# Performance work log

Hardware: AMD Instinct MI355X
Metric: run time of the kernel (lower is better)

## Reference

```python
import jax, jax.numpy as jnp
import numpy as np

D_MODEL = 1024
N_HEADS = 16
D_K = D_MODEL // N_HEADS  # 64
N_CLASSES = 32
S_LEN = 16   # synonyms per class
BATCH = 32
T_LEN = 512  # key/value sequence length


def setup_inputs() -> dict:
    key = jax.random.key(0)
    k1, k2, k3, k4, k5, k6 = jax.random.split(key, 6)
    Q = jax.random.normal(k1, (N_CLASSES, S_LEN, D_MODEL), dtype=jnp.float32)
    H = jax.random.normal(k2, (BATCH, T_LEN, D_MODEL), dtype=jnp.float32)
    ql = jax.random.normal(k3, (N_CLASSES, D_MODEL), dtype=jnp.float32)
    # torch Linear weights are (out_features, in_features), init N(0, 0.001)
    WQ_w = 0.001 * jax.random.normal(k4, (D_MODEL, D_MODEL), dtype=jnp.float32)
    WK_w = 0.001 * jax.random.normal(k5, (D_MODEL, D_MODEL), dtype=jnp.float32)
    WV_w = 0.001 * jax.random.normal(k6, (D_MODEL, D_MODEL), dtype=jnp.float32)
    return {"Q": Q, "H": H, "ql": ql, "WQ_w": WQ_w, "WK_w": WK_w, "WV_w": WV_w}


def reference(Q, H, ql, WQ_w, WK_w, WV_w):
    c, s, d = Q.shape
    b, t, _ = H.shape
    nh, dk = N_HEADS, D_K
    # projections (torch Linear: x @ W.T)
    q_s = (Q @ WQ_w.T).reshape(c, s, nh, dk).transpose(0, 2, 1, 3)   # czsh
    k_s = (H @ WK_w.T).reshape(b, t, nh, dk).transpose(0, 2, 1, 3)   # bzth
    Wql = ql @ WV_w.T                                                # ch
    Hh = H.reshape(b, t, nh, dk).transpose(0, 2, 1, 3)               # bzth
    WK = jnp.tanh(k_s)
    K = jnp.tanh(Hh)
    # scores: (b, c, z, s, t)
    scores = jnp.einsum('bzth,czsh->bczst', WK, q_s)
    attn = jax.nn.softmax(scores, axis=-1)
    # context: (b, c, z, s, h)
    context = jnp.einsum('bzth,bczst->bczsh', K, attn)
    # AvgPool3d((1, s, 1)) + squeeze(-2): mean over s -> (b, c, z, h)
    ctx = context.mean(axis=3).reshape(b, c, nh * dk)                # (b, c, d_model)
    output = jnp.einsum('bch,ch->bc', ctx, Wql)
    return output
```

## Files before the change

### kernel.cpp

```cpp
#include <hip/hip_runtime.h>
#include <hip/hip_bf16.h>
#include <math.h>

#define D_MODEL 1024
#define N_HEADS 16
#define D_K 64
#define N_CLASSES 32
#define S_LEN 16
#define BATCH 32
#define T_LEN 512

typedef __bf16 bf16_t;
typedef bf16_t bf16x8 __attribute__((ext_vector_type(8)));
typedef float f32x4 __attribute__((ext_vector_type(4)));
typedef long lx2 __attribute__((ext_vector_type(2)));

__device__ inline unsigned short f2bf(float f) {
    unsigned int u = __float_as_uint(f);
    unsigned int r = (u + 0x7FFFu + ((u >> 16) & 1u)) >> 16;
    return (unsigned short)r;
}
__device__ inline float fast_tanh(float x) {
    float e = __expf(2.0f * x);
    return (e - 1.0f) * __builtin_amdgcn_rcpf(e + 1.0f);
}
__device__ inline float4 fast_tanh4(float4 v) {
    return make_float4(fast_tanh(v.x), fast_tanh(v.y), fast_tanh(v.z), fast_tanh(v.w));
}
__device__ inline float dot4(float4 a, float4 b) {
    return a.x * b.x + a.y * b.y + a.z * b.z + a.w * b.w;
}
__device__ inline float exp2_fast(float x) {
    float r;
    asm("v_exp_f32 %0, %1" : "=v"(r) : "v"(x));
    return r;
}
__device__ inline int pack_fp8x4(float4 v) {
    int p = __builtin_amdgcn_cvt_pk_fp8_f32(v.x, v.y, 0, false);
    p = __builtin_amdgcn_cvt_pk_fp8_f32(v.z, v.w, p, true);
    return p;
}
__device__ inline bf16x8 bf8_from_f32(const float* p) {
    float4 a = *(const float4*)p;
    float4 b = *(const float4*)(p + 4);
    union { bf16x8 v; unsigned short s[8]; } u;
    u.s[0] = f2bf(a.x); u.s[1] = f2bf(a.y); u.s[2] = f2bf(a.z); u.s[3] = f2bf(a.w);
    u.s[4] = f2bf(b.x); u.s[5] = f2bf(b.y); u.s[6] = f2bf(b.z); u.s[7] = f2bf(b.w);
    return u.v;
}

__device__ inline void async16(void* lds, const void* g) {
    __builtin_amdgcn_global_load_lds(
        (const __attribute__((address_space(1))) unsigned int*)g,
        (__attribute__((address_space(3))) unsigned int*)lds, 16, 0, 0);
}

__global__ __launch_bounds__(256) void prep_kernel(
    const float* __restrict__ H, int* __restrict__ Hf8,
    const float* __restrict__ WK, int* __restrict__ WKf8,
    const float4* __restrict__ Q, ushort4* __restrict__ Qb,
    const float4* __restrict__ WQ, ushort4* __restrict__ WQb,
    const float* __restrict__ ql, const float* __restrict__ WV,
    float* __restrict__ wql)
{
    __shared__ __align__(16) char psm[25600];
    const int bid = blockIdx.x;
    const int tid = threadIdx.x;
    if (bid < 256) {
        float4 (*qls)[16] = (float4(*)[16])psm;
        float4 (*WVs)[17] = (float4(*)[17])(psm + 8192);
        const int n0 = (bid & 15) * 64;
        const int k0 = (bid >> 4) * 64;
        for (int i = tid; i < 512; i += 256)
            qls[i >> 4][i & 15] = *(const float4*)(ql + (size_t)(i >> 4) * D_MODEL + k0 + (i & 15) * 4);
        for (int i = tid; i < 1024; i += 256)
            WVs[i >> 4][i & 15] = *(const float4*)(WV + (size_t)(n0 + (i >> 4)) * D_MODEL + k0 + (i & 15) * 4);
        __syncthreads();

        const int n = tid & 63;
        const int c0 = (tid >> 6) * 8;
        float acc[8] = {};
        for (int kq = 0; kq < 16; kq++) {
            const float4 wv = WVs[n][kq];
#pragma unroll
            for (int c = 0; c < 8; c++) acc[c] += dot4(qls[c0 + c][kq], wv);
        }
#pragma unroll
        for (int c = 0; c < 8; c++)
            atomicAdd(&wql[(size_t)(c0 + c) * D_MODEL + n0 + n], acc[c]);
    } else if (bid < 17664) {
        int i = (bid - 256) * 256 + tid;
        const float* in; int* out; float s;
        if (i < 4194304) { in = H; out = Hf8; s = 1.0f; }
        else { i -= 4194304; in = WK; out = WKf8; s = 512.0f; }
        const int p = i << 2;
        const int blk = p >> 10;
        const int pos = p & 1023;
        const int rb = blk >> 4, kb = blk & 15;
        const int q = pos >> 4;
        const int quad = q >> 4, l16 = q & 15;
        const int o = pos & 15;
        const int kh = o >> 3, b0 = o & 7;
        const int r = rb * 16 + l16;
        const int k = kb * 64 + kh * 32 + quad * 8 + b0;
        float4 v = *(const float4*)(in + (size_t)r * 1024 + k);
        v.x *= s; v.y *= s; v.z *= s; v.w *= s;
        out[i] = pack_fp8x4(v);
    } else {
        int i = (bid - 17664) * 256 + tid;
        const float4* in; ushort4* out; float s;
        if (i < 131072) { in = Q + i; out = Qb + i; s = 1.4426950408889634f; }
        else { i -= 131072; in = WQ + i; out = WQb + i; s = 1.0f; }
        float4 v = *in;
        ushort4 o;
        o.x = f2bf(v.x * s); o.y = f2bf(v.y * s); o.z = f2bf(v.z * s); o.w = f2bf(v.w * s);
        *out = o;
    }
}

__global__ __launch_bounds__(256) void gemms_kernel(
    const unsigned char* __restrict__ A8, const unsigned char* __restrict__ B8,
    unsigned short* __restrict__ wkt_b,
    const unsigned short* __restrict__ Qb, const unsigned short* __restrict__ WQb,
    unsigned short* __restrict__ qproj_b,
    const float* __restrict__ H, const float* __restrict__ wql,
    float* __restrict__ kv)
{
    __shared__ __align__(16) char smem[33280];
    const int bid = blockIdx.x;
    const int tid = threadIdx.x;
    const int wid = tid >> 6;
    const int lane = tid & 63;
    const int quad = lane >> 4;
    const int l16 = lane & 15;

    if (bid < 1024) {
        unsigned char* As = (unsigned char*)smem;
        unsigned char* Bs = (unsigned char*)smem + 8192;
        const int m0 = (bid & 127) * 128;
        const int n0 = (bid >> 7) * 128;
        const int wm = (wid >> 1) * 64;
        const int wn = (wid & 1) * 64;
        const int stA = wm >> 4;
        const int stB = wn >> 4;
        const int st = wid;
        const int cl = lane * 16;

        f32x4 acc[4][4] = {};
        const unsigned char* Ab = A8 + ((size_t)(m0 >> 4) * 16) * 1024;
        const unsigned char* Bb = B8 + ((size_t)(n0 >> 4) * 16) * 1024;

        for (int kb = 0; kb < 16; kb++) {
            async16(&As[tid * 16],        Ab + ((size_t)st * 16 + kb) * 1024 + cl);
            async16(&As[4096 + tid * 16], Ab + ((size_t)(st + 4) * 16 + kb) * 1024 + cl);
            async16(&Bs[tid * 16],        Bb + ((size_t)st * 16 + kb) * 1024 + cl);
            async16(&Bs[4096 + tid * 16], Bb + ((size_t)(st + 4) * 16 + kb) * 1024 + cl);
            __syncthreads();

            lx2 a8[4], b8[4];
#pragma unroll
            for (int mt = 0; mt < 4; mt++)
                a8[mt] = *(const lx2*)&As[(stA + mt) * 1024 + lane * 16];
#pragma unroll
            for (int nt = 0; nt < 4; nt++)
                b8[nt] = *(const lx2*)&Bs[(stB + nt) * 1024 + lane * 16];
#pragma unroll
            for (int mt = 0; mt < 4; mt++)
#pragma unroll
                for (int nt = 0; nt < 4; nt++) {
                    acc[mt][nt] = __builtin_amdgcn_mfma_f32_16x16x32_fp8_fp8(
                        a8[mt].x, b8[nt].x, acc[mt][nt], 0, 0, 0);
                    acc[mt][nt] = __builtin_amdgcn_mfma_f32_16x16x32_fp8_fp8(
                        a8[mt].y, b8[nt].y, acc[mt][nt], 0, 0, 0);
                }
            __syncthreads();
        }

#pragma unroll
        for (int mt = 0; mt < 4; mt++)
#pragma unroll
            for (int nt = 0; nt < 4; nt++)
#pragma unroll
                for (int r = 0; r < 4; r++) {
                    const int row = m0 + wm + mt * 16 + quad * 4 + r;
                    const int col = n0 + wn + nt * 16 + l16;
                    wkt_b[(size_t)row * 1024 + col] =
                        f2bf(fast_tanh(acc[mt][nt][r] * (1.0f / 512.0f)));
                }
    } else if (bid < 1056) {
        unsigned short* As = (unsigned short*)smem;
        unsigned short* Bs = (unsigned short*)(smem + 8192);
        const int q = bid - 1024;
        const int m0 = (q & 3) * 128;
        const int n0 = (q >> 2) * 128;
        const int wm = (wid >> 1) * 64;
        const int wn = (wid & 1) * 64;

        f32x4 acc[4][4] = {};
        const int r0 = tid >> 2;
        const int cc0 = (tid & 3) * 8;

        for (int k0 = 0; k0 < 1024; k0 += 32) {
            async16(&As[tid * 8],        Qb  + (size_t)(m0 + r0) * 1024 + k0 + cc0);
            async16(&As[2048 + tid * 8], Qb  + (size_t)(m0 + 64 + r0) * 1024 + k0 + cc0);
            async16(&Bs[tid * 8],        WQb + (size_t)(n0 + r0) * 1024 + k0 + cc0);
            async16(&Bs[2048 + tid * 8], WQb + (size_t)(n0 + 64 + r0) * 1024 + k0 + cc0);
            __syncthreads();

            bf16x8 af[4], bfr[4];
#pragma unroll
            for (int mt = 0; mt < 4; mt++)
                af[mt] = *(const bf16x8*)&As[(wm + mt * 16 + l16) * 32 + quad * 8];
#pragma unroll
            for (int nt = 0; nt < 4; nt++)
                bfr[nt] = *(const bf16x8*)&Bs[(wn + nt * 16 + l16) * 32 + quad * 8];
#pragma unroll
            for (int mt = 0; mt < 4; mt++)
#pragma unroll
                for (int nt = 0; nt < 4; nt++)
                    acc[mt][nt] = __builtin_amdgcn_mfma_f32_16x16x32_bf16(
                        af[mt], bfr[nt], acc[mt][nt], 0, 0, 0);
            __syncthreads();
        }

#pragma unroll
        for (int mt = 0; mt < 4; mt++)
#pragma unroll
            for (int nt = 0; nt < 4; nt++)
#pragma unroll
                for (int r = 0; r < 4; r++) {
                    const int row = m0 + wm + mt * 16 + quad * 4 + r;
                    const int col = n0 + wn + nt * 16 + l16;
                    qproj_b[(size_t)row * 1024 + col] = f2bf(acc[mt][nt][r]);
                }
    } else {
        unsigned short* Ks = (unsigned short*)smem;
        float* kvt = (float*)(smem + 16384);
        const int q = bid - 1056;
        const int chunk = q & 127;
        const int z = q >> 7;
        const int b = chunk >> 2;
        const int t0 = (chunk & 3) * 128;

#pragma unroll
        for (int it = 0; it < 8; it++) {
            const int idx = it * 256 + tid;
            const int row = idx >> 4;
            const int c4 = (idx & 15) * 4;
            float4 v = *(const float4*)(H + ((size_t)b * T_LEN + t0 + row) * D_MODEL + z * D_K + c4);
            v = fast_tanh4(v);
            ushort4 o;
            o.x = f2bf(v.x); o.y = f2bf(v.y); o.z = f2bf(v.z); o.w = f2bf(v.w);
            *(ushort4*)&Ks[row * 64 + c4] = o;
        }
        bf16x8 bfr[2][2];
#pragma unroll
        for (int ct = 0; ct < 2; ct++)
#pragma unroll
            for (int kh = 0; kh < 2; kh++)
                bfr[ct][kh] = bf8_from_f32(wql +
                    (size_t)(ct * 16 + l16) * D_MODEL + z * D_K + kh * 32 + quad * 8);
        __syncthreads();

        const int wt = wid * 32;
        f32x4 acc[2][2] = {};
#pragma unroll
        for (int tt = 0; tt < 2; tt++) {
            const bf16x8 a0 = *(const bf16x8*)&Ks[(wt + tt * 16 + l16) * 64 + quad * 8];
            const bf16x8 a1 = *(const bf16x8*)&Ks[(wt + tt * 16 + l16) * 64 + 32 + quad * 8];
#pragma unroll
            for (int ct = 0; ct < 2; ct++) {
                acc[tt][ct] = __builtin_amdgcn_mfma_f32_16x16x32_bf16(a0, bfr[ct][0], acc[tt][ct], 0, 0, 0);
                acc[tt][ct] = __builtin_amdgcn_mfma_f32_16x16x32_bf16(a1, bfr[ct][1], acc[tt][ct], 0, 0, 0);
            }
        }
#pragma unroll
        for (int tt = 0; tt < 2; tt++)
#pragma unroll
            for (int ct = 0; ct < 2; ct++)
#pragma unroll
                for (int r = 0; r < 4; r++)
                    kvt[(wt + tt * 16 + quad * 4 + r) * 33 + ct * 16 + l16] = acc[tt][ct][r];
        __syncthreads();

        float* outb = kv + (((size_t)b * 16 + z) * 32) * 512 + t0;
#pragma unroll
        for (int it = 0; it < 4; it++) {
            const int idx = it * 256 + tid;
            const int c = idx >> 5;
            const int tq = (idx & 31) * 4;
            float4 v = make_float4(kvt[(tq + 0) * 33 + c], kvt[(tq + 1) * 33 + c],
                                   kvt[(tq + 2) * 33 + c], kvt[(tq + 3) * 33 + c]);
            *(float4*)(outb + (size_t)c * 512 + tq) = v;
        }
    }
}

__global__ __launch_bounds__(512, 4) void attn_mfma(
    const unsigned short* __restrict__ qproj, const unsigned short* __restrict__ wkt,
    const float* __restrict__ kv, float* __restrict__ part)
{
    __shared__ unsigned short wkts[512 * 64];
    const int z = blockIdx.x;
    const int b = blockIdx.y;
    const int tid = threadIdx.x;
    const int wid = tid >> 6;
    const int lane = tid & 63;
    const int quad = lane >> 4;
    const int l16 = lane & 15;

    const unsigned short* wb = wkt + (size_t)(b * T_LEN) * D_MODEL + z * D_K;
#pragma unroll
    for (int it = 0; it < 8; it++) {
        const int chunk = it * 512 + tid;
        const int row = chunk >> 3;
        const int c = chunk & 7;
        async16(&wkts[chunk * 8], wb + (size_t)row * D_MODEL + ((c ^ (row & 7)) * 8));
    }

    bf16x8 af[4][2];
#pragma unroll
    for (int ct = 0; ct < 4; ct++)
#pragma unroll
        for (int kh = 0; kh < 2; kh++)
            af[ct][kh] = *(const bf16x8*)(qproj +
                (size_t)((wid * 4 + ct) * 16 + l16) * D_MODEL + z * D_K + kh * 32 + quad * 8);
    __syncthreads();

    float den[4][4], num[4][4];
#pragma unroll
    for (int ct = 0; ct < 4; ct++)
#pragma unroll
        for (int r = 0; r < 4; r++) { den[ct][r] = 0.f; num[ct][r] = 0.f; }

    const float* kvp = kv + (((size_t)b * 16 + z) * 32 + wid * 4) * 512 + l16;
    float kc[4];
#pragma unroll
    for (int ct = 0; ct < 4; ct++) kc[ct] = kvp[ct * 512];

    const int x0 = (quad ^ (l16 & 7)) * 8;
    const int x1 = ((quad ^ 4) ^ (l16 & 7)) * 8;
    for (int nt = 0; nt < 32; nt++) {
        float kn[4];
#pragma unroll
        for (int ct = 0; ct < 4; ct++) kn[ct] = kvp[ct * 512 + (nt + 1) * 16];
        const int rbase = (nt * 16 + l16) * 64;
        const bf16x8 b0 = *(const bf16x8*)&wkts[rbase + x0];
        const bf16x8 b1 = *(const bf16x8*)&wkts[rbase + x1];
        f32x4 a4[4];
        __builtin_amdgcn_s_setprio(1);
#pragma unroll
        for (int ct = 0; ct < 4; ct++) {
            f32x4 a = {};
            a = __builtin_amdgcn_mfma_f32_16x16x32_bf16(af[ct][0], b0, a, 0, 0, 0);
            a = __builtin_amdgcn_mfma_f32_16x16x32_bf16(af[ct][1], b1, a, 0, 0, 0);
            a4[ct] = a;
        }
        __builtin_amdgcn_s_setprio(0);
#pragma unroll
        for (int ct = 0; ct < 4; ct++)
#pragma unroll
            for (int r = 0; r < 4; r++) {
                const float e = exp2_fast(a4[ct][r]);
                den[ct][r] += e;
                num[ct][r] += e * kc[ct];
            }
#pragma unroll
        for (int ct = 0; ct < 4; ct++) kc[ct] = kn[ct];
    }

#pragma unroll
    for (int ct = 0; ct < 4; ct++) {
        float s = 0.f;
#pragma unroll
        for (int r = 0; r < 4; r++) {
            float d = den[ct][r], n = num[ct][r];
#pragma unroll
            for (int off = 1; off < 16; off <<= 1) {
                d += __shfl_xor(d, off, 64);
                n += __shfl_xor(n, off, 64);
            }
            s += n / d;
        }
        s += __shfl_xor(s, 16, 64);
        s += __shfl_xor(s, 32, 64);
        if (lane == 0)
            part[((size_t)(b * N_CLASSES) + wid * 4 + ct) * 16 + z] = s;
    }
}

__global__ __launch_bounds__(256) void attn_reduce(
    const float* __restrict__ part, float* __restrict__ out)
{
    const int i = blockIdx.x * 256 + threadIdx.x;
    const float* p = part + (size_t)i * 16;
    float s = 0.f;
#pragma unroll
    for (int zz = 0; zz < 16; zz++) s += p[zz];
    out[i] = s * (1.0f / 16.0f);
}

extern "C" void kernel_launch(void* const* d_in, const int* in_sizes, int n_in,
                              void* d_out, int out_size, void* d_ws, size_t ws_size,
                              hipStream_t stream)
{
    const float* Q  = (const float*)d_in[0];
    const float* H  = (const float*)d_in[1];
    const float* ql = (const float*)d_in[2];
    const float* WQ = (const float*)d_in[3];
    const float* WK = (const float*)d_in[4];
    const float* WV = (const float*)d_in[5];
    float* out = (float*)d_out;

    char* ws = (char*)d_ws;
    unsigned char*  Hf8     = (unsigned char*)(ws);
    unsigned short* Qb      = (unsigned short*)(ws + (size_t)25165824);
    unsigned short* WQb     = (unsigned short*)(ws + (size_t)26214400);
    unsigned short* qproj_b = (unsigned short*)(ws + (size_t)28311552);
    float*          part    = (float*)(ws + (size_t)30408704);
    float*          wqlb    = (float*)(ws + (size_t)31457280);
    unsigned short* wkt_b   = (unsigned short*)(ws + (size_t)33554432);
    float*          kv      = (float*)(ws + (size_t)67108864);
    unsigned char*  WKf8    = (unsigned char*)(ws + (size_t)100663296);

    dim3 thr(256);
    hipMemsetAsync(wqlb, 0, (size_t)N_CLASSES * D_MODEL * sizeof(float), stream);
    prep_kernel<<<dim3(19200), thr, 0, stream>>>(
        H, (int*)Hf8, WK, (int*)WKf8,
        (const float4*)Q, (ushort4*)Qb,
        (const float4*)WQ, (ushort4*)WQb,
        ql, WV, wqlb);
    gemms_kernel<<<dim3(3104), thr, 0, stream>>>(
        Hf8, WKf8, wkt_b, Qb, WQb, qproj_b, H, wqlb, kv);
    attn_mfma<<<dim3(16, 32), dim3(512), 0, stream>>>(qproj_b, wkt_b, kv, part);
    attn_reduce<<<dim3(4), thr, 0, stream>>>(part, out);
}
```

Measured before the change: 207.0 us.

## Stage fp8 repack through LDS and double-buffer fp8 GEMM tiles

```diff
diff --git a/kernel.cpp b/kernel.cpp
--- a/kernel.cpp
+++ b/kernel.cpp
@@ -88,26 +88,37 @@
 #pragma unroll
         for (int c = 0; c < 8; c++)
             atomicAdd(&wql[(size_t)(c0 + c) * D_MODEL + n0 + n], acc[c]);
-    } else if (bid < 17664) {
-        int i = (bid - 256) * 256 + tid;
-        const float* in; int* out; float s;
-        if (i < 4194304) { in = H; out = Hf8; s = 1.0f; }
-        else { i -= 4194304; in = WK; out = WKf8; s = 512.0f; }
-        const int p = i << 2;
-        const int blk = p >> 10;
-        const int pos = p & 1023;
-        const int rb = blk >> 4, kb = blk & 15;
-        const int q = pos >> 4;
-        const int quad = q >> 4, l16 = q & 15;
-        const int o = pos & 15;
-        const int kh = o >> 3, b0 = o & 7;
-        const int r = rb * 16 + l16;
-        const int k = kb * 64 + kh * 32 + quad * 8 + b0;
-        float4 v = *(const float4*)(in + (size_t)r * 1024 + k);
-        v.x *= s; v.y *= s; v.z *= s; v.w *= s;
-        out[i] = pack_fp8x4(v);
+    } else if (bid < 4608) {
+        float (*L)[260] = (float(*)[260])psm;
+        int j = bid - 256;
+        const float* in; int* out; float s; int jj;
+        if (j < 4096) { in = H; out = Hf8; s = 1.0f; jj = j; }
+        else { in = WK; out = WKf8; s = 512.0f; jj = j - 4096; }
+        const int rb = jj >> 2;
+        const int kb0 = (jj & 3) * 4;
+        const float* base = in + (size_t)rb * 16 * 1024 + kb0 * 64;
+#pragma unroll
+        for (int it = 0; it < 4; it++) {
+            const int idx = it * 256 + tid;
+            const int row = idx >> 6;
+            const int c0 = (idx & 63) * 4;
+            *(float4*)&L[row][c0] = *(const float4*)(base + (size_t)row * 1024 + c0);
+        }
+        __syncthreads();
+        const int quad = tid >> 6;
+        const int l16 = (tid >> 2) & 15;
+        const int kh = (tid & 3) >> 1;
+        const int b0 = (tid & 1) * 4;
+        const int klb = kh * 32 + quad * 8 + b0;
+        int* outp = out + (size_t)jj * 1024 + tid;
+#pragma unroll
+        for (int p = 0; p < 4; p++) {
+            float4 v = *(const float4*)&L[l16][p * 64 + klb];
+            v.x *= s; v.y *= s; v.z *= s; v.w *= s;
+            outp[p * 256] = pack_fp8x4(v);
+        }
     } else {
-        int i = (bid - 17664) * 256 + tid;
+        int i = (bid - 4608) * 256 + tid;
         const float4* in; ushort4* out; float s;
         if (i < 131072) { in = Q + i; out = Qb + i; s = 1.4426950408889634f; }
         else { i -= 131072; in = WQ + i; out = WQb + i; s = 1.0f; }
@@ -136,7 +147,7 @@
 
     if (bid < 1024) {
         unsigned char* As = (unsigned char*)smem;
-        unsigned char* Bs = (unsigned char*)smem + 8192;
+        unsigned char* Bs = (unsigned char*)smem + 16384;
         const int m0 = (bid & 127) * 128;
         const int n0 = (bid >> 7) * 128;
         const int wm = (wid >> 1) * 64;
@@ -150,20 +161,26 @@
         const unsigned char* Ab = A8 + ((size_t)(m0 >> 4) * 16) * 1024;
         const unsigned char* Bb = B8 + ((size_t)(n0 >> 4) * 16) * 1024;
 
+        auto stage = [&](int buf, int kb) {
+            async16(&As[buf * 8192 + tid * 16],        Ab + ((size_t)st * 16 + kb) * 1024 + cl);
+            async16(&As[buf * 8192 + 4096 + tid * 16], Ab + ((size_t)(st + 4) * 16 + kb) * 1024 + cl);
+            async16(&Bs[buf * 8192 + tid * 16],        Bb + ((size_t)st * 16 + kb) * 1024 + cl);
+            async16(&Bs[buf * 8192 + 4096 + tid * 16], Bb + ((size_t)(st + 4) * 16 + kb) * 1024 + cl);
+        };
+
+        stage(0, 0);
+        __syncthreads();
         for (int kb = 0; kb < 16; kb++) {
-            async16(&As[tid * 16],        Ab + ((size_t)st * 16 + kb) * 1024 + cl);
-            async16(&As[4096 + tid * 16], Ab + ((size_t)(st + 4) * 16 + kb) * 1024 + cl);
-            async16(&Bs[tid * 16],        Bb + ((size_t)st * 16 + kb) * 1024 + cl);
-            async16(&Bs[4096 + tid * 16], Bb + ((size_t)(st + 4) * 16 + kb) * 1024 + cl);
-            __syncthreads();
+            const int cur = kb & 1;
+            if (kb < 15) stage(cur ^ 1, kb + 1);
 
             lx2 a8[4], b8[4];
 #pragma unroll
             for (int mt = 0; mt < 4; mt++)
-                a8[mt] = *(const lx2*)&As[(stA + mt) * 1024 + lane * 16];
+                a8[mt] = *(const lx2*)&As[cur * 8192 + (stA + mt) * 1024 + lane * 16];
 #pragma unroll
             for (int nt = 0; nt < 4; nt++)
-                b8[nt] = *(const lx2*)&Bs[(stB + nt) * 1024 + lane * 16];
+                b8[nt] = *(const lx2*)&Bs[cur * 8192 + (stB + nt) * 1024 + lane * 16];
 #pragma unroll
             for (int mt = 0; mt < 4; mt++)
 #pragma unroll
@@ -425,7 +442,7 @@
 
     dim3 thr(256);
     hipMemsetAsync(wqlb, 0, (size_t)N_CLASSES * D_MODEL * sizeof(float), stream);
-    prep_kernel<<<dim3(19200), thr, 0, stream>>>(
+    prep_kernel<<<dim3(6144), thr, 0, stream>>>(
         H, (int*)Hf8, WK, (int*)WKf8,
         (const float4*)Q, (ushort4*)Qb,
         (const float4*)WQ, (ushort4*)WQb,
```

Result: faster. 201.3 us (-2.7%).
